# Optimization experiments

Measured on AMD Instinct MI355X. Metric: run time of the kernel, lower is better.

## Reference

```python
import jax, jax.numpy as jnp
import numpy as np

D, K, B, IMG, NCH = 128, 512, 8, 128, 3


def adder2d(x, w, k, stride, pad):
    # AdderNet L1 'convolution': y[b,co,l] = -sum_p |patch[b,p,l] - w[co,p]|
    # x: [B,C,H,W], w: [Cout, C*k*k]
    p = jax.lax.conv_general_dilated_patches(x, (k, k), (stride, stride), [(pad, pad), (pad, pad)])
    Bb, P, Ho, Wo = p.shape
    p = p.reshape(Bb, P, Ho * Wo)  # [B, C*k*k, L]
    def one(wc):  # wc: [P] -> [B, L]; sequential over Cout to bound memory
        return -jnp.sum(jnp.abs(p - wc[None, :, None]), axis=1)
    o = jax.lax.map(one, w)  # [Cout, B, L]
    return jnp.transpose(o, (1, 0, 2)).reshape(Bb, w.shape[0], Ho, Wo)


def bn(x, g, b, eps=1e-5):
    # eval-mode BatchNorm2d with running_mean=0, running_var=1
    s = g * jax.lax.rsqrt(jnp.asarray(1.0 + eps, x.dtype))
    return x * s[None, :, None, None] + b[None, :, None, None]


def conv2d(x, w, b, pad):
    y = jax.lax.conv_general_dilated(x, w, (1, 1), [(pad, pad), (pad, pad)],
                                     dimension_numbers=('NCHW', 'OIHW', 'NCHW'))
    return y + b[None, :, None, None]


def up2x(x):  # nn.Upsample(scale_factor=2, bilinear, align_corners=False)
    Bb, C, H, W = x.shape
    return jax.image.resize(x, (Bb, C, 2 * H, 2 * W), method='bilinear')


def adder_resblock(x, w1, w2, g, b):
    # [ReLU, adder3x3, BN, ReLU, adder1x1] + residual
    h = jax.nn.relu(x)
    h = adder2d(h, w1, 3, 1, 1)
    h = bn(h, g, b)
    h = jax.nn.relu(h)
    h = adder2d(h, w2, 1, 1, 0)
    return x + h


def conv_resblock(x, w1, b1, w2, b2):
    # [ReLU, conv3x3, ReLU, conv1x1] + residual (bn=False in decoder)
    h = jax.nn.relu(x)
    h = conv2d(h, w1, b1, 1)
    h = jax.nn.relu(h)
    h = conv2d(h, w2, b2, 0)
    return x + h


def vq_forward(z_e, E):
    # NearestEmbed: E is [d, k]
    Bb, C, H, W = z_e.shape
    flat = jnp.transpose(z_e, (0, 2, 3, 1)).reshape(-1, C)  # [N, d]
    d2 = (jnp.sum(flat * flat, axis=1, keepdims=True)
          - 2.0 * (flat @ E) + jnp.sum(E * E, axis=0)[None, :])  # [N, k]
    argmin = jnp.argmin(d2, axis=1)  # [N]
    q = jnp.take(E.T, argmin, axis=0)  # [N, d]
    # weight_sg=True path: straight-through to z_e, no grad to E
    zq_flat = flat + jax.lax.stop_gradient(q - flat)
    z_q = jnp.transpose(zq_flat.reshape(Bb, H, W, C), (0, 3, 1, 2))
    # emb path: z_e detached, grad flows to E through the gather
    emb = jnp.transpose(q.reshape(Bb, H, W, C), (0, 3, 1, 2))
    return z_q, emb, argmin.reshape(Bb, H, W)


def reference(x, we1, we2, ae1_w1, ae1_w2, ae2_w1, ae2_w2, bn_gamma, bn_beta,
              emb_weight, rd1_w1, rd1_b1, rd1_w2, rd1_b2, rd2_w1, rd2_b1,
              rd2_w2, rd2_b2, cd1_w, cd1_b, cd2_w, cd2_b):
    g, b = bn_gamma, bn_beta
    h = adder2d(x, we1, 4, 2, 1)
    h = jax.nn.relu(bn(h, g[0], b[0]))
    h = adder2d(h, we2, 4, 2, 1)
    h = jax.nn.relu(bn(h, g[1], b[1]))
    h = adder_resblock(h, ae1_w1, ae1_w2, g[2], b[2])
    h = bn(h, g[3], b[3])
    h = adder_resblock(h, ae2_w1, ae2_w2, g[4], b[4])
    z_e = bn(h, g[5], b[5])  # bne4 (gamma = 1/40)

    z_q, emb, argmin = vq_forward(z_e, emb_weight)

    y = conv_resblock(z_q, rd1_w1, rd1_b1, rd1_w2, rd1_b2)
    y = bn(y, g[6], b[6])
    y = conv_resblock(y, rd2_w1, rd2_b1, rd2_w2, rd2_b2)
    y = up2x(y)
    y = conv2d(y, cd1_w, cd1_b, 1)
    y = jax.nn.relu(bn(y, g[7], b[7]))
    y = up2x(y)
    y = conv2d(y, cd2_w, cd2_b, 1)
    y = jnp.tanh(y)
    return (y, z_e, emb, argmin)


def setup_inputs() -> dict:
    key = jax.random.key(0)
    ks = jax.random.split(key, 16)
    f = lambda k, shp: (0.02 * jax.random.normal(k, shp)).astype(jnp.float32)
    inp = {}
    inp['x'] = jax.random.normal(ks[0], (B, NCH, IMG, IMG), jnp.float32)
    inp['we1'] = f(ks[1], (D, NCH * 16))       # adder 4x4 s2
    inp['we2'] = f(ks[2], (D, D * 16))
    inp['ae1_w1'] = f(ks[3], (D, D * 9))       # adder 3x3
    inp['ae1_w2'] = f(ks[4], (D, D))           # adder 1x1
    inp['ae2_w1'] = f(ks[5], (D, D * 9))
    inp['ae2_w2'] = f(ks[6], (D, D))
    inp['bn_gamma'] = jnp.ones((8, D), jnp.float32).at[5].set(1.0 / 40.0)
    inp['bn_beta'] = jnp.zeros((8, D), jnp.float32)
    inp['emb_weight'] = f(ks[7], (D, K))
    inp['rd1_w1'] = f(ks[8], (D, D, 3, 3)); inp['rd1_b1'] = jnp.zeros(D, jnp.float32)
    inp['rd1_w2'] = f(ks[9], (D, D, 1, 1)); inp['rd1_b2'] = jnp.zeros(D, jnp.float32)
    inp['rd2_w1'] = f(ks[10], (D, D, 3, 3)); inp['rd2_b1'] = jnp.zeros(D, jnp.float32)
    inp['rd2_w2'] = f(ks[11], (D, D, 1, 1)); inp['rd2_b2'] = jnp.zeros(D, jnp.float32)
    inp['cd1_w'] = f(ks[12], (D, D, 3, 3)); inp['cd1_b'] = jnp.zeros(D, jnp.float32)
    inp['cd2_w'] = f(ks[13], (NCH, D, 3, 3)); inp['cd2_b'] = jnp.zeros(NCH, jnp.float32)
    return inp
```

## Files before the change

kernel.cpp:

```cpp
#include <hip/hip_runtime.h>
#include <math.h>

constexpr int Dc = 128;
constexpr int Kc = 512;
constexpr int Bc = 8;

template<int ISADD, int K, int STRIDE, int PAD, int IT, int EPI, int CIN, int CH,
         int OUT_ROWS, int WOUT, int WIN, int HIN, int HOUT, int COBW>
__global__ __launch_bounds__(256)
void lds_layer(const float* __restrict__ x, const float* __restrict__ w,
               const float* __restrict__ bias,
               const float* __restrict__ itG, const float* __restrict__ itB,
               const float* __restrict__ res,
               const float* __restrict__ rG, const float* __restrict__ rB,
               const float* __restrict__ oG, const float* __restrict__ oB,
               float* __restrict__ out) {
  constexpr int PW = 2;
  constexpr int KK = K * K;
  constexpr int SPAN = (PW - 1) * STRIDE + K;
  constexpr int IN_ROWS = (OUT_ROWS - 1) * STRIDE + K;
  constexpr int WPAD = (WOUT - 1) * STRIDE + K;
  constexpr int WLDS = (WPAD + 3) & ~3;
  constexpr int PGW = WOUT / PW;
  static_assert(OUT_ROWS * PGW == 64, "one wave covers the pixel tile");
  constexpr int NCG = Dc / (4 * COBW);
  constexpr int NBAND = HOUT / OUT_ROWS;
  constexpr int W4 = WIN / 4;
  constexpr int NELEM4 = CH * IN_ROWS * W4;
  constexpr int NIT4 = (NELEM4 + 255) / 256;
  constexpr bool EXACT = (NELEM4 % 256) == 0;
  const float r15 = rsqrtf(1.0f + 1e-5f);

  __shared__ alignas(16) float lds[CH][IN_ROWS][WLDS];

  int tid = threadIdx.x;
  int gb = blockIdx.x;
  int cg = gb / (Bc * NBAND);
  int rem = gb % (Bc * NBAND);
  int band = rem % NBAND;
  int b = rem / NBAND;
  int wv = __builtin_amdgcn_readfirstlane(tid >> 6);
  int lane = tid & 63;
  int co0 = cg * (4 * COBW) + wv * COBW;
  int pr = lane / PGW, pc = lane % PGW;
  int oh = band * OUT_ROWS + pr;
  int ow0 = pc * PW;
  int yi0 = band * OUT_ROWS * STRIDE - PAD;

  for (int e = tid; e < CH * IN_ROWS * WLDS; e += 256) ((float*)lds)[e] = 0.f;

  float acc[PW][COBW];
#pragma unroll
  for (int p = 0; p < PW; ++p)
#pragma unroll
    for (int j = 0; j < COBW; ++j)
      acc[p][j] = ISADD ? 0.f : bias[co0 + j];

  const float* xb = x + (long)b * CIN * HIN * WIN;
  float4 rbuf[NIT4];

  auto stage = [&](int c0) {
#pragma unroll
    for (int it = 0; it < NIT4; ++it) {
      int e = it * 256 + tid;
      if (!EXACT && e >= NELEM4) break;
      int c4 = e % W4;
      int r = (e / W4) % IN_ROWS;
      int ch = e / (W4 * IN_ROWS);
      int yi = yi0 + r;
      float4 v = make_float4(0.f, 0.f, 0.f, 0.f);
      if (yi >= 0 && yi < HIN) {
        v = *(const float4*)&xb[((long)(c0 + ch) * HIN + yi) * WIN + 4 * c4];
        if (IT == 1) {
          v.x = fmaxf(v.x, 0.f); v.y = fmaxf(v.y, 0.f);
          v.z = fmaxf(v.z, 0.f); v.w = fmaxf(v.w, 0.f);
        }
        if (IT == 2) {
          float sc = itG[c0 + ch] * r15, bc = itB[c0 + ch];
          v.x = fmaxf(fmaf(v.x, sc, bc), 0.f);
          v.y = fmaxf(fmaf(v.y, sc, bc), 0.f);
          v.z = fmaxf(fmaf(v.z, sc, bc), 0.f);
          v.w = fmaxf(fmaf(v.w, sc, bc), 0.f);
        }
      }
      rbuf[it] = v;
    }
  };
  auto towrite = [&]() {
#pragma unroll
    for (int it = 0; it < NIT4; ++it) {
      int e = it * 256 + tid;
      if (!EXACT && e >= NELEM4) break;
      int c4 = e % W4;
      int r = (e / W4) % IN_ROWS;
      int ch = e / (W4 * IN_ROWS);
      float* p = &lds[ch][r][4 * c4 + PAD];
      float4 v = rbuf[it];
      p[0] = v.x; p[1] = v.y; p[2] = v.z; p[3] = v.w;
    }
  };

  stage(0);
  for (int c0 = 0; c0 < CIN; c0 += CH) {
    __syncthreads();
    towrite();
    __syncthreads();
    if (c0 + CH < CIN) stage(c0 + CH);
    for (int ch = 0; ch < CH; ++ch) {
      float vbuf[K][SPAN];
#pragma unroll
      for (int kh = 0; kh < K; ++kh) {
        const float* rp0 = &lds[ch][pr * STRIDE + kh][ow0 * STRIDE];
        if constexpr (SPAN == 6 && (PW * STRIDE) % 4 == 0) {
          float4 a = *(const float4*)rp0;
          float2 c2 = *(const float2*)(rp0 + 4);
          vbuf[kh][0] = a.x; vbuf[kh][1] = a.y; vbuf[kh][2] = a.z;
          vbuf[kh][3] = a.w; vbuf[kh][4] = c2.x; vbuf[kh][5] = c2.y;
        } else if constexpr (SPAN == 4 && (PW * STRIDE) % 2 == 0) {
          float2 a = *(const float2*)rp0;
          float2 c2 = *(const float2*)(rp0 + 2);
          vbuf[kh][0] = a.x; vbuf[kh][1] = a.y;
          vbuf[kh][2] = c2.x; vbuf[kh][3] = c2.y;
        } else if constexpr (SPAN == 2 && (PW * STRIDE) % 2 == 0) {
          float2 a = *(const float2*)rp0;
          vbuf[kh][0] = a.x; vbuf[kh][1] = a.y;
        } else {
#pragma unroll
          for (int s = 0; s < SPAN; ++s) vbuf[kh][s] = rp0[s];
        }
      }
      const float* wc = w + ((long)co0 * CIN + (c0 + ch)) * KK;
#pragma unroll
      for (int kh = 0; kh < K; ++kh)
#pragma unroll
        for (int kw = 0; kw < K; ++kw)
#pragma unroll
          for (int j = 0; j < COBW; ++j) {
            float ww = wc[(long)j * CIN * KK + kh * K + kw];
#pragma unroll
            for (int p = 0; p < PW; ++p) {
              float v = vbuf[kh][p * STRIDE + kw];
              if (ISADD) acc[p][j] += fabsf(v - ww);
              else       acc[p][j] = fmaf(v, ww, acc[p][j]);
            }
          }
    }
  }

  long obase = ((long)(b * Dc + co0) * HOUT + oh) * WOUT + ow0;
  float* ob = out + obase;
  const float* rp = (EPI == 2 || EPI == 3 || EPI == 6) ? res + obase : nullptr;
  constexpr long hw = (long)HOUT * WOUT;
#pragma unroll
  for (int j = 0; j < COBW; ++j) {
    float og = 0.f, obb = 0.f, rg = 0.f, rbb = 0.f;
    if (EPI == 1 || EPI == 6) { og = oG[co0 + j] * r15; obb = oB[co0 + j]; }
    if (EPI == 3 || EPI == 6) { rg = rG[co0 + j] * r15; rbb = rB[co0 + j]; }
#pragma unroll
    for (int p = 0; p < PW; ++p) {
      float val = ISADD ? -acc[p][j] : acc[p][j];
      if (EPI == 1) val = fmaxf(fmaf(val, og, obb), 0.f);
      if (EPI == 2) val = rp[j * hw + p] + val;
      if (EPI == 3) val = fmaf(rp[j * hw + p], rg, rbb) + val;
      if (EPI == 5) val = fmaxf(val, 0.f);
      if (EPI == 6) val = fmaf(fmaf(rp[j * hw + p], rg, rbb) + val, og, obb);
      ob[j * hw + p] = val;
    }
  }
}

__device__ __forceinline__ void up_coef(int p, int H, int& i0, int& i1, float& w0, float& w1) {
  int m = p >> 1;
  if ((p & 1) == 0) { i0 = (m > 0) ? m - 1 : 0; i1 = m; w0 = 0.25f; w1 = 0.75f; }
  else              { i0 = m; i1 = (m + 1 < H) ? m + 1 : H - 1; w0 = 0.75f; w1 = 0.25f; }
}

__global__ void up2x_kernel(const float* __restrict__ in, float* __restrict__ out,
                            int C, int H, int W) {
  int H2 = 2 * H, W2 = 2 * W;
  int i = blockIdx.x * blockDim.x + threadIdx.x;
  int total = Bc * C * H2 * W2;
  if (i >= total) return;
  int ow = i % W2; int t = i / W2;
  int oh = t % H2; t /= H2;
  int c = t % C; int b = t / C;
  int y0, y1, x0, x1; float wy0, wy1, wx0, wx1;
  up_coef(oh, H, y0, y1, wy0, wy1);
  up_coef(ow, W, x0, x1, wx0, wx1);
  const float* p = in + (b * C + c) * H * W;
  float v = wy0 * (wx0 * p[y0 * W + x0] + wx1 * p[y0 * W + x1])
          + wy1 * (wx0 * p[y1 * W + x0] + wx1 * p[y1 * W + x1]);
  out[i] = v;
}

__global__ __launch_bounds__(256)
void conv3x3_up_tanh_quad(const float* __restrict__ x, const float* __restrict__ w,
                          const float* __restrict__ bias, float* __restrict__ out,
                          int Hs, int Ws, int Cout) {
  constexpr int CIN = Dc;
  int H2 = 2 * Hs, W2 = 2 * Ws;
  int nq = Hs * Ws;
  int i = blockIdx.x * blockDim.x + threadIdx.x;
  int total = Bc * Cout * nq;
  if (i >= total) return;
  int q = i % nq; int t = i / nq;
  int co = t % Cout; int b = t / Cout;
  int n = q % Ws, m = q / Ws;
  int rows[3] = { (m > 0) ? m - 1 : 0, m, (m + 1 < Hs) ? m + 1 : Hs - 1 };
  int cols[3] = { (n > 0) ? n - 1 : 0, n, (n + 1 < Ws) ? n + 1 : Ws - 1 };
  float rv[4] = { (2 * m - 1 >= 0) ? 1.f : 0.f, 1.f, 1.f, (2 * m + 2 < H2) ? 1.f : 0.f };
  float cv[4] = { (2 * n - 1 >= 0) ? 1.f : 0.f, 1.f, 1.f, (2 * n + 2 < W2) ? 1.f : 0.f };
  float bco = bias[co];
  float acc[4] = { bco, bco, bco, bco };
  const float* xb = x + b * CIN * nq;
  const float* wb = w + co * CIN * 9;
  for (int c = 0; c < CIN; ++c) {
    const float* xc = xb + c * nq;
    float s[3][3];
#pragma unroll
    for (int a = 0; a < 3; ++a)
#pragma unroll
      for (int e = 0; e < 3; ++e) s[a][e] = xc[rows[a] * Ws + cols[e]];
    float rb[4][3];
#pragma unroll
    for (int e = 0; e < 3; ++e) {
      rb[0][e] = fmaf(0.75f, s[0][e], 0.25f * s[1][e]);
      rb[1][e] = fmaf(0.25f, s[0][e], 0.75f * s[1][e]);
      rb[2][e] = fmaf(0.75f, s[1][e], 0.25f * s[2][e]);
      rb[3][e] = fmaf(0.25f, s[1][e], 0.75f * s[2][e]);
    }
    float u[4][4];
#pragma unroll
    for (int di = 0; di < 4; ++di) {
      float rm = rv[di];
      u[di][0] = fmaf(0.75f, rb[di][0], 0.25f * rb[di][1]) * rm * cv[0];
      u[di][1] = fmaf(0.25f, rb[di][0], 0.75f * rb[di][1]) * rm * cv[1];
      u[di][2] = fmaf(0.75f, rb[di][1], 0.25f * rb[di][2]) * rm * cv[2];
      u[di][3] = fmaf(0.25f, rb[di][1], 0.75f * rb[di][2]) * rm * cv[3];
    }
    const float* wc = wb + c * 9;
#pragma unroll
    for (int kh = 0; kh < 3; ++kh)
#pragma unroll
      for (int kw = 0; kw < 3; ++kw) {
        float ww = wc[kh * 3 + kw];
        acc[0] = fmaf(u[kh][kw],         ww, acc[0]);
        acc[1] = fmaf(u[kh][kw + 1],     ww, acc[1]);
        acc[2] = fmaf(u[kh + 1][kw],     ww, acc[2]);
        acc[3] = fmaf(u[kh + 1][kw + 1], ww, acc[3]);
      }
  }
  float* ob = out + (b * Cout + co) * H2 * W2 + (2 * m) * W2 + 2 * n;
  ob[0] = tanhf(acc[0]);      ob[1] = tanhf(acc[1]);
  ob[W2] = tanhf(acc[2]);     ob[W2 + 1] = tanhf(acc[3]);
}

__global__ void vq_e2_kernel(const float* __restrict__ E, float* __restrict__ e2) {
  int k = blockIdx.x * blockDim.x + threadIdx.x;
  if (k >= Kc) return;
  float s = 0.f;
  for (int d = 0; d < Dc; ++d) { float v = E[d * Kc + k]; s += v * v; }
  e2[k] = s;
}

__global__ __launch_bounds__(256)
void vq_kernel8(const float* __restrict__ z_e, const float* __restrict__ E,
                const float* __restrict__ e2,
                float* __restrict__ emb, float* __restrict__ argmin_out) {
  constexpr int HW = 1024;
  __shared__ float f[8][Dc];
  __shared__ float d2s[8][256];
  __shared__ int   ks[8][256];
  int tid = threadIdx.x;
  int n0 = blockIdx.x * 8;
  int b = n0 >> 10;
  int rem = n0 & 1023;
  const float* zb = z_e + (long)b * Dc * HW + rem;
#pragma unroll
  for (int i = 0; i < 4; ++i) {
    int e = i * 256 + tid;
    int p = e & 7, d = e >> 3;
    f[p][d] = zb[d * HW + p];
  }
  __syncthreads();
  float f2 = 0.f;
  if (tid < 8) {
    for (int d = 0; d < Dc; ++d) f2 += f[tid][d] * f[tid][d];
    d2s[tid][0] = f2;
  }
  __syncthreads();
  float f2v[8];
#pragma unroll
  for (int p = 0; p < 8; ++p) f2v[p] = d2s[p][0];
  __syncthreads();

  float best[8]; int bk[8];
#pragma unroll
  for (int p = 0; p < 8; ++p) { best[p] = 3.4e38f; bk[p] = 0; }
  for (int kk = tid; kk < Kc; kk += 256) {
    float dot[8];
#pragma unroll
    for (int p = 0; p < 8; ++p) dot[p] = 0.f;
    for (int d = 0; d < Dc; ++d) {
      float ed = E[d * Kc + kk];
#pragma unroll
      for (int p = 0; p < 8; ++p) dot[p] = fmaf(f[p][d], ed, dot[p]);
    }
    float e2k = e2[kk];
#pragma unroll
    for (int p = 0; p < 8; ++p) {
      float d2 = f2v[p] - 2.f * dot[p] + e2k;
      if (d2 < best[p] || (d2 == best[p] && kk < bk[p])) { best[p] = d2; bk[p] = kk; }
    }
  }
#pragma unroll
  for (int p = 0; p < 8; ++p) { d2s[p][tid] = best[p]; ks[p][tid] = bk[p]; }
  __syncthreads();
  for (int s = 128; s > 0; s >>= 1) {
    if (tid < s) {
#pragma unroll
      for (int p = 0; p < 8; ++p) {
        float ob = d2s[p][tid + s]; int ok = ks[p][tid + s];
        if (ob < d2s[p][tid] || (ob == d2s[p][tid] && ok < ks[p][tid])) {
          d2s[p][tid] = ob; ks[p][tid] = ok;
        }
      }
    }
    __syncthreads();
  }
  if (tid < 8) argmin_out[n0 + tid] = (float)ks[tid][0];
  float* eb = emb + (long)b * Dc * HW + rem;
#pragma unroll
  for (int i = 0; i < 4; ++i) {
    int e = i * 256 + tid;
    int p = e & 7, d = e >> 3;
    eb[d * HW + p] = E[d * Kc + ks[p][0]];
  }
}

extern "C" void kernel_launch(void* const* d_in, const int* in_sizes, int n_in,
                              void* d_out, int out_size, void* d_ws, size_t ws_size,
                              hipStream_t stream) {
  const float* x      = (const float*)d_in[0];
  const float* we1    = (const float*)d_in[1];
  const float* we2    = (const float*)d_in[2];
  const float* ae1_w1 = (const float*)d_in[3];
  const float* ae1_w2 = (const float*)d_in[4];
  const float* ae2_w1 = (const float*)d_in[5];
  const float* ae2_w2 = (const float*)d_in[6];
  const float* bn_g   = (const float*)d_in[7];
  const float* bn_b   = (const float*)d_in[8];
  const float* embw   = (const float*)d_in[9];
  const float* rd1_w1 = (const float*)d_in[10];
  const float* rd1_b1 = (const float*)d_in[11];
  const float* rd1_w2 = (const float*)d_in[12];
  const float* rd1_b2 = (const float*)d_in[13];
  const float* rd2_w1 = (const float*)d_in[14];
  const float* rd2_b1 = (const float*)d_in[15];
  const float* rd2_w2 = (const float*)d_in[16];
  const float* rd2_b2 = (const float*)d_in[17];
  const float* cd1_w  = (const float*)d_in[18];
  const float* cd1_b  = (const float*)d_in[19];
  const float* cd2_w  = (const float*)d_in[20];
  const float* cd2_b  = (const float*)d_in[21];

  const float* g0 = bn_g + 0 * Dc; const float* b0 = bn_b + 0 * Dc;
  const float* g1 = bn_g + 1 * Dc; const float* b1 = bn_b + 1 * Dc;
  const float* g2 = bn_g + 2 * Dc; const float* b2 = bn_b + 2 * Dc;
  const float* g3 = bn_g + 3 * Dc; const float* b3 = bn_b + 3 * Dc;
  const float* g4 = bn_g + 4 * Dc; const float* b4 = bn_b + 4 * Dc;
  const float* g5 = bn_g + 5 * Dc; const float* b5 = bn_b + 5 * Dc;
  const float* g6 = bn_g + 6 * Dc; const float* b6 = bn_b + 6 * Dc;
  const float* g7 = bn_g + 7 * Dc; const float* b7 = bn_b + 7 * Dc;

  float* W64a = (float*)d_ws;
  float* W64b = W64a + 4194304;
  float* Wa   = W64b + 4194304;
  float* Wb   = Wa + 1048576;
  float* Wc   = Wb + 1048576;
  float* e2b  = W64b;

  float* out_y   = (float*)d_out;
  float* out_ze  = out_y  + 393216;
  float* out_emb = out_ze + 1048576;
  float* out_am  = out_emb + 1048576;

  const int TB = 256;
  auto nb = [](int n) { return (n + 255) / 256; };
  const int N64 = Bc * Dc * 64 * 64;
  const float* nul = nullptr;

  const int G32c2 = 16 * Bc * 8;
  const int G32c4 = 8 * Bc * 8;
  const int G64c4 = 8 * Bc * 32;
  const int G64c8 = 4 * Bc * 32;

  lds_layer<1,4,2,1, 0,1, 3,3, 2,64,128,128,64, 4><<<G64c4, TB, 0, stream>>>(
      x, we1, nul, nul, nul, nul, nul, nul, g0, b0, W64a);
  lds_layer<1,4,2,1, 0,1, Dc,8, 4,32,64,64,32, 2><<<G32c2, TB, 0, stream>>>(
      W64a, we2, nul, nul, nul, nul, nul, nul, g1, b1, Wa);
  lds_layer<1,3,1,1, 0,1, Dc,32, 4,32,32,32,32, 2><<<G32c2, TB, 0, stream>>>(
      Wa, ae1_w1, nul, nul, nul, nul, nul, nul, g2, b2, Wb);
  lds_layer<1,1,1,0, 0,2, Dc,64, 4,32,32,32,32, 4><<<G32c4, TB, 0, stream>>>(
      Wb, ae1_w2, nul, nul, nul, Wa, nul, nul, nul, nul, Wc);
  lds_layer<1,3,1,1, 2,1, Dc,32, 4,32,32,32,32, 2><<<G32c2, TB, 0, stream>>>(
      Wc, ae2_w1, nul, g3, b3, nul, nul, nul, g4, b4, Wb);
  lds_layer<1,1,1,0, 0,6, Dc,64, 4,32,32,32,32, 4><<<G32c4, TB, 0, stream>>>(
      Wb, ae2_w2, nul, nul, nul, Wc, g3, b3, g5, b5, out_ze);

  vq_e2_kernel<<<2, 256, 0, stream>>>(embw, e2b);
  vq_kernel8<<<Bc * 1024 / 8, 256, 0, stream>>>(out_ze, embw, e2b, out_emb, out_am);

  lds_layer<0,3,1,1, 1,5, Dc,32, 4,32,32,32,32, 2><<<G32c2, TB, 0, stream>>>(
      out_emb, rd1_w1, rd1_b1, nul, nul, nul, nul, nul, nul, nul, Wb);
  lds_layer<0,1,1,0, 0,2, Dc,64, 4,32,32,32,32, 4><<<G32c4, TB, 0, stream>>>(
      Wb, rd1_w2, rd1_b2, nul, nul, out_emb, nul, nul, nul, nul, Wa);
  lds_layer<0,3,1,1, 2,5, Dc,32, 4,32,32,32,32, 2><<<G32c2, TB, 0, stream>>>(
      Wa, rd2_w1, rd2_b1, g6, b6, nul, nul, nul, nul, nul, Wb);
  lds_layer<0,1,1,0, 0,3, Dc,64, 4,32,32,32,32, 4><<<G32c4, TB, 0, stream>>>(
      Wb, rd2_w2, rd2_b2, nul, nul, Wa, g6, b6, nul, nul, Wc);

  up2x_kernel<<<nb(N64), TB, 0, stream>>>(Wc, W64a, Dc, 32, 32);
  lds_layer<0,3,1,1, 0,1, Dc,16, 2,64,64,64,64, 8><<<G64c8, TB, 0, stream>>>(
      W64a, cd1_w, cd1_b, nul, nul, nul, nul, nul, g7, b7, W64b);

  conv3x3_up_tanh_quad<<<nb(Bc * 3 * 64 * 64), TB, 0, stream>>>(W64b, cd2_w, cd2_b, out_y, 64, 64, 3);
}
```

Before: 877.2 us.

## Double-buffer LDS input tiles and preload per-channel weights into registers

Switches the LDS input tile to two buffers, so the next channel chunk is written to LDS while the current one is consumed, leaving one barrier per chunk instead of two. Channel chunk sizes are halved so the doubled LDS footprint stays about the same. Each output channel's KK weights are now loaded into a register array before the inner loop instead of being read per tap. This overlaps global loads with compute at the cost of more registers and more loop iterations.

```diff
diff --git a/kernel.cpp b/kernel.cpp
--- a/kernel.cpp
+++ b/kernel.cpp
@@ -29,9 +29,11 @@
   constexpr int NELEM4 = CH * IN_ROWS * W4;
   constexpr int NIT4 = (NELEM4 + 255) / 256;
   constexpr bool EXACT = (NELEM4 % 256) == 0;
+  constexpr bool MULTI = (CIN > CH);
+  constexpr int NBUF = MULTI ? 2 : 1;
   const float r15 = rsqrtf(1.0f + 1e-5f);
 
-  __shared__ alignas(16) float lds[CH][IN_ROWS][WLDS];
+  __shared__ alignas(16) float lds[NBUF][CH][IN_ROWS][WLDS];
 
   int tid = threadIdx.x;
   int gb = blockIdx.x;
@@ -46,8 +48,6 @@
   int oh = band * OUT_ROWS + pr;
   int ow0 = pc * PW;
   int yi0 = band * OUT_ROWS * STRIDE - PAD;
-
-  for (int e = tid; e < CH * IN_ROWS * WLDS; e += 256) ((float*)lds)[e] = 0.f;
 
   float acc[PW][COBW];
 #pragma unroll
@@ -86,7 +86,7 @@
       rbuf[it] = v;
     }
   };
-  auto towrite = [&]() {
+  auto towrite = [&](int bi) {
 #pragma unroll
     for (int it = 0; it < NIT4; ++it) {
       int e = it * 256 + tid;
@@ -94,23 +94,32 @@
       int c4 = e % W4;
       int r = (e / W4) % IN_ROWS;
       int ch = e / (W4 * IN_ROWS);
-      float* p = &lds[ch][r][4 * c4 + PAD];
+      float* p = &lds[bi][ch][r][4 * c4 + PAD];
       float4 v = rbuf[it];
       p[0] = v.x; p[1] = v.y; p[2] = v.z; p[3] = v.w;
     }
   };
 
   stage(0);
+  for (int e = tid; e < NBUF * CH * IN_ROWS * WLDS; e += 256) ((float*)lds)[e] = 0.f;
+  __syncthreads();
+  towrite(0);
+  if (MULTI) stage(CH);
+  __syncthreads();
+
+  int cur = 0;
   for (int c0 = 0; c0 < CIN; c0 += CH) {
-    __syncthreads();
-    towrite();
-    __syncthreads();
-    if (c0 + CH < CIN) stage(c0 + CH);
+    bool more = MULTI && (c0 + CH < CIN);
+    int nxt = (NBUF == 2) ? (cur ^ 1) : 0;
+    if (more) {
+      towrite(nxt);
+      if (c0 + 2 * CH < CIN) stage(c0 + 2 * CH);
+    }
     for (int ch = 0; ch < CH; ++ch) {
       float vbuf[K][SPAN];
 #pragma unroll
       for (int kh = 0; kh < K; ++kh) {
-        const float* rp0 = &lds[ch][pr * STRIDE + kh][ow0 * STRIDE];
+        const float* rp0 = &lds[cur][ch][pr * STRIDE + kh][ow0 * STRIDE];
         if constexpr (SPAN == 6 && (PW * STRIDE) % 4 == 0) {
           float4 a = *(const float4*)rp0;
           float2 c2 = *(const float2*)(rp0 + 4);
@@ -131,12 +140,16 @@
       }
       const float* wc = w + ((long)co0 * CIN + (c0 + ch)) * KK;
 #pragma unroll
-      for (int kh = 0; kh < K; ++kh)
-#pragma unroll
-        for (int kw = 0; kw < K; ++kw)
-#pragma unroll
-          for (int j = 0; j < COBW; ++j) {
-            float ww = wc[(long)j * CIN * KK + kh * K + kw];
+      for (int j = 0; j < COBW; ++j) {
+        const float* wj = wc + (long)j * CIN * KK;
+        float wvr[KK];
+#pragma unroll
+        for (int t = 0; t < KK; ++t) wvr[t] = wj[t];
+#pragma unroll
+        for (int kh = 0; kh < K; ++kh)
+#pragma unroll
+          for (int kw = 0; kw < K; ++kw) {
+            float ww = wvr[kh * K + kw];
 #pragma unroll
             for (int p = 0; p < PW; ++p) {
               float v = vbuf[kh][p * STRIDE + kw];
@@ -144,6 +157,11 @@
               else       acc[p][j] = fmaf(v, ww, acc[p][j]);
             }
           }
+      }
+    }
+    if (more) {
+      __syncthreads();
+      cur = nxt;
     }
   }
 
@@ -397,27 +415,27 @@
 
   lds_layer<1,4,2,1, 0,1, 3,3, 2,64,128,128,64, 4><<<G64c4, TB, 0, stream>>>(
       x, we1, nul, nul, nul, nul, nul, nul, g0, b0, W64a);
-  lds_layer<1,4,2,1, 0,1, Dc,8, 4,32,64,64,32, 2><<<G32c2, TB, 0, stream>>>(
+  lds_layer<1,4,2,1, 0,1, Dc,4, 4,32,64,64,32, 2><<<G32c2, TB, 0, stream>>>(
       W64a, we2, nul, nul, nul, nul, nul, nul, g1, b1, Wa);
-  lds_layer<1,3,1,1, 0,1, Dc,32, 4,32,32,32,32, 2><<<G32c2, TB, 0, stream>>>(
+  lds_layer<1,3,1,1, 0,1, Dc,16, 4,32,32,32,32, 2><<<G32c2, TB, 0, stream>>>(
       Wa, ae1_w1, nul, nul, nul, nul, nul, nul, g2, b2, Wb);
-  lds_layer<1,1,1,0, 0,2, Dc,64, 4,32,32,32,32, 4><<<G32c4, TB, 0, stream>>>(
+  lds_layer<1,1,1,0, 0,2, Dc,32, 4,32,32,32,32, 4><<<G32c4, TB, 0, stream>>>(
       Wb, ae1_w2, nul, nul, nul, Wa, nul, nul, nul, nul, Wc);
-  lds_layer<1,3,1,1, 2,1, Dc,32, 4,32,32,32,32, 2><<<G32c2, TB, 0, stream>>>(
+  lds_layer<1,3,1,1, 2,1, Dc,16, 4,32,32,32,32, 2><<<G32c2, TB, 0, stream>>>(
       Wc, ae2_w1, nul, g3, b3, nul, nul, nul, g4, b4, Wb);
-  lds_layer<1,1,1,0, 0,6, Dc,64, 4,32,32,32,32, 4><<<G32c4, TB, 0, stream>>>(
+  lds_layer<1,1,1,0, 0,6, Dc,32, 4,32,32,32,32, 4><<<G32c4, TB, 0, stream>>>(
       Wb, ae2_w2, nul, nul, nul, Wc, g3, b3, g5, b5, out_ze);
 
   vq_e2_kernel<<<2, 256, 0, stream>>>(embw, e2b);
   vq_kernel8<<<Bc * 1024 / 8, 256, 0, stream>>>(out_ze, embw, e2b, out_emb, out_am);
 
-  lds_layer<0,3,1,1, 1,5, Dc,32, 4,32,32,32,32, 2><<<G32c2, TB, 0, stream>>>(
+  lds_layer<0,3,1,1, 1,5, Dc,16, 4,32,32,32,32, 2><<<G32c2, TB, 0, stream>>>(
       out_emb, rd1_w1, rd1_b1, nul, nul, nul, nul, nul, nul, nul, Wb);
-  lds_layer<0,1,1,0, 0,2, Dc,64, 4,32,32,32,32, 4><<<G32c4, TB, 0, stream>>>(
+  lds_layer<0,1,1,0, 0,2, Dc,32, 4,32,32,32,32, 4><<<G32c4, TB, 0, stream>>>(
       Wb, rd1_w2, rd1_b2, nul, nul, out_emb, nul, nul, nul, nul, Wa);
-  lds_layer<0,3,1,1, 2,5, Dc,32, 4,32,32,32,32, 2><<<G32c2, TB, 0, stream>>>(
+  lds_layer<0,3,1,1, 2,5, Dc,16, 4,32,32,32,32, 2><<<G32c2, TB, 0, stream>>>(
       Wa, rd2_w1, rd2_b1, g6, b6, nul, nul, nul, nul, nul, Wb);
-  lds_layer<0,1,1,0, 0,3, Dc,64, 4,32,32,32,32, 4><<<G32c4, TB, 0, stream>>>(
+  lds_layer<0,1,1,0, 0,3, Dc,32, 4,32,32,32,32, 4><<<G32c4, TB, 0, stream>>>(
       Wb, rd2_w2, rd2_b2, nul, nul, Wa, g6, b6, nul, nul, Wc);
 
   up2x_kernel<<<nb(N64), TB, 0, stream>>>(Wc, W64a, Dc, 32, 32);
```

New measurement: 1.155 ms. 31.7% more time.
